# Kernel tuning notes

Hardware: AMD Instinct MI355X
Metric: run time of the kernel (lower is better)

Reference implementation:

```python
import jax, jax.numpy as jnp
import numpy as np

P, A = 8, 65536            # poses, atoms per pose
N = P * A                  # total atoms
N1 = N + 1                 # kin nodes (node 0 = virtual root)


def _local_hts(dofs):
    """Per-node local homogeneous transform from bond DOFs.
    dofs[:,0]=phi (torsion), dofs[:,1]=theta (bond angle), dofs[:,2]=d (length).
    M = Rz(phi) @ Ry(theta) @ Trans_x(d)   (NeRF-style internal coordinates)."""
    phi, theta, d = dofs[:, 0], dofs[:, 1], dofs[:, 2]
    cp, sp = jnp.cos(phi), jnp.sin(phi)
    ct, st = jnp.cos(theta), jnp.sin(theta)
    z = jnp.zeros_like(phi)
    o = jnp.ones_like(phi)
    # R = Rz(phi) @ Ry(theta)
    r00, r01, r02 = cp * ct, -sp, cp * st
    r10, r11, r12 = sp * ct, cp, sp * st
    r20, r21, r22 = -st, z, ct
    # t = R @ [d,0,0]
    t0, t1, t2 = d * r00, d * r10, d * r20
    M = jnp.stack([
        jnp.stack([r00, r01, r02, t0], -1),
        jnp.stack([r10, r11, r12, t1], -1),
        jnp.stack([r20, r21, r22, t2], -1),
        jnp.stack([z, z, z, o], -1),
    ], -2)  # [N1,4,4]
    return M


def setup_inputs() -> dict:
    rng = np.random.default_rng(0)
    # tree: each node's parent is 1..4 nodes back (topologically sorted), root self-parented
    parents = np.zeros(N1, np.int32)
    idx = np.arange(1, N1)
    parents[1:] = np.maximum(idx - 1 - rng.integers(0, 4, size=N), 0).astype(np.int32)
    # kinforest.id: permutation mapping kin node (1..N) -> flat atom index
    kin_id = rng.permutation(N).astype(np.int32)
    # base DOFs (detached full_dofs): realistic bond geometry
    base = np.zeros((N1, 4), np.float32)
    base[:, 1] = rng.uniform(1.5, 2.2, N1)          # theta
    base[:, 2] = rng.normal(1.53, 0.02, N1)         # bond length
    masked = rng.uniform(-np.pi, np.pi, N1).astype(np.float32)  # torsion params
    bond_w = rng.uniform(0.5, 1.5, (P, A - 1)).astype(np.float32)
    pose_coords = np.zeros((P, A, 3), np.float32)
    return {
        "masked_dofs": jnp.asarray(masked),
        "base_dofs": jnp.asarray(base),
        "pose_coords": jnp.asarray(pose_coords),
        "bond_w": jnp.asarray(bond_w),
        "parents": jnp.asarray(parents),
        "kin_id": jnp.asarray(kin_id),
    }


def reference(masked_dofs, base_dofs, pose_coords, bond_w, parents, kin_id):
    # 1) write optimizable DOFs into full DOF tensor (dof_mask = torsion column)
    dofs = base_dofs.at[:, 0].set(masked_dofs)
    # 2) per-node local transforms; root = identity
    M = _local_hts(dofs)
    M = M.at[0].set(jnp.eye(4, dtype=M.dtype))
    # 3) forwardKin: compose parent->child transforms via pointer doubling
    n_iters = int(np.ceil(np.log2(N1)))
    def body(carry, _):
        G, p = carry
        G = jnp.einsum('nij,njk->nik', G[p], G)
        return (G, p[p]), None
    (G, _), _ = jax.lax.scan(body, (M, parents), None, length=n_iters)
    kincoords = G[1:, :3, 3]  # [N,3] global positions (skip root)
    # 4) scatter kin coords back into pose-stack coordinates
    flat = pose_coords.reshape(-1, 3).at[kin_id].set(kincoords)
    coords = flat.reshape(pose_coords.shape)  # [P,A,3]
    # 5) whole-pose scoring: weighted bonded quadratic energy per pose
    d = coords[:, 1:] - coords[:, :-1]
    energy = jnp.sum(bond_w * jnp.sum(d * d, -1), axis=-1)  # [P]
    return energy
```

## Files before the change

kernel.cpp:

```cpp
#include <hip/hip_runtime.h>

#define N_TOT  524288
#define NN1    524289
#define PP     8
#define AA     65536
#define SEGLEN 64
#define NSEG   8193
#define CHUNK  64
#define NCHK   129
#define NE     (NCHK*4)

#define OFF_COORDS 0
#define OFF_NT   2097152
#define OFF_L1G  4194308
#define OFF_L1E  4587572
#define OFF_PREG 4620344
#define OFF_PREE 5013608
#define OFF_CLG  5046380
#define OFF_CLE  5052572

static __device__ __forceinline__ void set_ident(float* a){
  a[0]=1.f;a[1]=0.f;a[2]=0.f;a[3]=0.f;
  a[4]=0.f;a[5]=1.f;a[6]=0.f;a[7]=0.f;
  a[8]=0.f;a[9]=0.f;a[10]=1.f;a[11]=0.f;
}

static __device__ __forceinline__ void compose(const float* Aa, const float* B, float* O){
  #pragma unroll
  for(int r=0;r<3;r++){
    float a0=Aa[r*4+0],a1=Aa[r*4+1],a2=Aa[r*4+2],a3=Aa[r*4+3];
    O[r*4+0]=a0*B[0]+a1*B[4]+a2*B[8];
    O[r*4+1]=a0*B[1]+a1*B[5]+a2*B[9];
    O[r*4+2]=a0*B[2]+a1*B[6]+a2*B[10];
    O[r*4+3]=a0*B[3]+a1*B[7]+a2*B[11]+a3;
  }
}

static __device__ __forceinline__ void load12(const float4* b4, int idx, float* a){
  float4 x=b4[idx*3+0], y=b4[idx*3+1], z=b4[idx*3+2];
  a[0]=x.x;a[1]=x.y;a[2]=x.z;a[3]=x.w;
  a[4]=y.x;a[5]=y.y;a[6]=y.z;a[7]=y.w;
  a[8]=z.x;a[9]=z.y;a[10]=z.z;a[11]=z.w;
}
static __device__ __forceinline__ void store12(float4* b4, int idx, const float* a){
  b4[idx*3+0]=make_float4(a[0],a[1],a[2],a[3]);
  b4[idx*3+1]=make_float4(a[4],a[5],a[6],a[7]);
  b4[idx*3+2]=make_float4(a[8],a[9],a[10],a[11]);
}

static __device__ __forceinline__ void wave_scan(
    int w, int lane,
    const float* __restrict__ masked, const float4* __restrict__ base4,
    const int* __restrict__ parents,
    float G[12], int& pk)
{
  int i0 = w*SEGLEN;
  int i = i0 + lane;
  if(i == 0 || i >= NN1){
    set_ident(G); pk = 0xFF;
  } else {
    float4 b = base4[i];
    float phi = masked[i];
    float sp,cp,st,ct;
    __sincosf(phi,&sp,&cp);
    __sincosf(b.y,&st,&ct);
    float dd = b.z;
    G[0]=cp*ct; G[1]=-sp; G[2]=cp*st; G[3]=dd*G[0];
    G[4]=sp*ct; G[5]=cp;  G[6]=sp*st; G[7]=dd*G[4];
    G[8]=-st;   G[9]=0.f; G[10]=ct;   G[11]=dd*G[8];
    int rel = parents[i] - i0;
    pk = (rel >= 0) ? rel : (((rel+4)<<8) | 0xFF);
  }
  #pragma unroll
  for(int step=0; step<6; ++step){
    int ptr = pk & 0xFF;
    bool act = (ptr != 0xFF);
    int src = act ? ptr : lane;
    float g2[12];
    #pragma unroll
    for(int q=0;q<12;q++) g2[q] = __shfl(G[q], src, 64);
    int pk2 = __shfl(pk, src, 64);
    float ng[12];
    compose(g2, G, ng);
    #pragma unroll
    for(int q=0;q<12;q++) G[q] = act ? ng[q] : G[q];
    pk = act ? pk2 : pk;
  }
}

__global__ __launch_bounds__(1024) void fk1(
    const float* __restrict__ masked, const float4* __restrict__ base4,
    const int* __restrict__ parents,
    float4* __restrict__ L1G, int* __restrict__ L1E,
    float4* __restrict__ NT, float* __restrict__ out)
{
  if(blockIdx.x==0 && threadIdx.x < PP) out[threadIdx.x] = 0.f;
  int w = blockIdx.x*16 + (threadIdx.x>>6);
  if(w >= NSEG) return;
  int lane = threadIdx.x & 63;
  float G[12]; int pk;
  wave_scan(w, lane, masked, base4, parents, G, pk);
  int i = w*SEGLEN + lane;
  int tag = (pk>>8)&3;
  if(i < NN1){
    NT[i] = make_float4(G[3], G[7], G[11], __int_as_float(tag));
  }
  if(lane >= 60){
    int j = lane - 60;
    store12(L1G, w*4+j, G);
    L1E[w*4+j] = tag;
  }
}

__global__ __launch_bounds__(64) void fk2(
    const float4* __restrict__ L1G, const int* __restrict__ L1E,
    float4* __restrict__ PREG, int* __restrict__ PREE,
    float4* __restrict__ CLG, int* __restrict__ CLE)
{
  int g = blockIdx.x;
  int j = threadIdx.x;
  int s0 = g*CHUNK;
  int ns = min(CHUNK, NSEG - s0);
  int sj = s0 + min(j, ns-1);

  float A[4][12]; int at[4];
  #pragma unroll
  for(int t=0;t<4;t++){
    load12(L1G, sj*4+t, A[t]);
    at[t] = L1E[sj*4+t];
  }
  if(j >= ns){
    #pragma unroll
    for(int t=0;t<4;t++){ set_ident(A[t]); at[t]=t; }
  }

  #pragma unroll
  for(int step=0; step<6; ++step){
    int d = 1<<step;
    int src = (j >= d) ? (j - d) : j;
    float f[4][12]; int ft[4];
    #pragma unroll
    for(int t=0;t<4;t++){
      #pragma unroll
      for(int q=0;q<12;q++) f[t][q] = __shfl(A[t][q], src, 64);
      ft[t] = __shfl(at[t], src, 64);
    }
    bool act = (j >= d) && (j < ns);
    float nA[4][12]; int nt[4];
    #pragma unroll
    for(int t=0;t<4;t++){
      int tt = at[t];
      float sel[12];
      #pragma unroll
      for(int q=0;q<12;q++){
        float v01 = (tt&1) ? f[1][q] : f[0][q];
        float v23 = (tt&1) ? f[3][q] : f[2][q];
        sel[q] = (tt&2) ? v23 : v01;
      }
      compose(sel, A[t], nA[t]);
      int t01 = (tt&1) ? ft[1] : ft[0];
      int t23 = (tt&1) ? ft[3] : ft[2];
      nt[t] = (tt&2) ? t23 : t01;
    }
    #pragma unroll
    for(int t=0;t<4;t++){
      #pragma unroll
      for(int q=0;q<12;q++) A[t][q] = act ? nA[t][q] : A[t][q];
      at[t] = act ? nt[t] : at[t];
    }
  }

  if(j == 0){
    float I[12]; set_ident(I);
    #pragma unroll
    for(int t=0;t<4;t++){
      store12(PREG, s0*4+t, I);
      PREE[s0*4+t] = t;
    }
  }
  if(j < ns-1){
    #pragma unroll
    for(int t=0;t<4;t++){
      store12(PREG, (s0+j+1)*4+t, A[t]);
      PREE[(s0+j+1)*4+t] = at[t];
    }
  }
  if(j == ns-1){
    #pragma unroll
    for(int t=0;t<4;t++){
      store12(CLG, g*4+t, A[t]);
      CLE[g*4+t] = at[t];
    }
  }
}

__global__ __launch_bounds__(1024) void fk34(
    const int* __restrict__ kin, const float4* __restrict__ NT,
    const float4* __restrict__ PREG, const int* __restrict__ PREE,
    const float4* __restrict__ CLG, const int* __restrict__ CLE,
    float4* __restrict__ coords)
{
  __shared__ float Lg[NE*12];
  __shared__ int   Le[NE];
  float4* Lg4 = (float4*)Lg;
  int tid = threadIdx.x;

  if(tid < NE){
    float a[12]; load12(CLG, tid, a);
    Lg4[tid*3+0]=make_float4(a[0],a[1],a[2],a[3]);
    Lg4[tid*3+1]=make_float4(a[4],a[5],a[6],a[7]);
    Lg4[tid*3+2]=make_float4(a[8],a[9],a[10],a[11]);
    Le[tid]=CLE[tid];
  }
  __syncthreads();
  for(int d=1; d<NCHK; d<<=1){
    float ng[12]; int ne2=0;
    bool doit = (tid<NE) && ((tid>>2)>=d);
    if(doit){
      int myE = Le[tid];
      int pe = ((tid>>2)-d)*4 + myE;
      float own[12], pg[12];
      load12(Lg4, tid, own);
      load12(Lg4, pe, pg);
      compose(pg, own, ng);
      ne2 = Le[pe];
    }
    __syncthreads();
    if(doit){
      Lg4[tid*3+0]=make_float4(ng[0],ng[1],ng[2],ng[3]);
      Lg4[tid*3+1]=make_float4(ng[4],ng[5],ng[6],ng[7]);
      Lg4[tid*3+2]=make_float4(ng[8],ng[9],ng[10],ng[11]);
      Le[tid]=ne2;
    }
    __syncthreads();
  }

  int w = blockIdx.x*16 + (tid>>6);
  if(w >= NSEG) return;
  int lane = tid & 63;
  int i = w*SEGLEN + lane;
  if(i == 0 || i >= NN1) return;
  float4 nt = NT[i];
  int tag = __float_as_int(nt.w) & 3;
  int c = w >> 6;
  int e = PREE[w*4+tag];
  float bg[12], pg[12], A[12];
  if(c == 0){ set_ident(bg); }
  else { load12(Lg4, (c-1)*4+e, bg); }
  load12(PREG, w*4+tag, pg);
  compose(bg, pg, A);
  float x = A[0]*nt.x + A[1]*nt.y + A[2]*nt.z  + A[3];
  float y = A[4]*nt.x + A[5]*nt.y + A[6]*nt.z  + A[7];
  float z = A[8]*nt.x + A[9]*nt.y + A[10]*nt.z + A[11];
  coords[kin[i-1]] = make_float4(x, y, z, 0.f);
}

__global__ void fk5(const float4* __restrict__ coords, const float* __restrict__ bw,
                    float* __restrict__ out)
{
  int p = blockIdx.x >> 5;
  int sub = blockIdx.x & 31;
  int a0 = sub * 2048;
  int aend = min(a0 + 2048, AA - 1);
  float sum = 0.f;
  for(int a = a0 + (int)threadIdx.x; a < aend; a += 256){
    int r = p*AA + a;
    float4 c0 = coords[r], c1 = coords[r+1];
    float dx = c1.x-c0.x, dy = c1.y-c0.y, dz = c1.z-c0.z;
    sum += bw[p*(AA-1)+a]*(dx*dx+dy*dy+dz*dz);
  }
  #pragma unroll
  for(int off=32;off>0;off>>=1) sum += __shfl_down(sum, off, 64);
  __shared__ float red[4];
  int lane = threadIdx.x & 63, wid = threadIdx.x >> 6;
  if(lane==0) red[wid]=sum;
  __syncthreads();
  if(threadIdx.x==0){
    float tot = red[0]+red[1]+red[2]+red[3];
    atomicAdd(&out[p], tot);
  }
}

extern "C" void kernel_launch(void* const* d_in, const int* in_sizes, int n_in,
                              void* d_out, int out_size, void* d_ws, size_t ws_size,
                              hipStream_t stream)
{
  const float*  masked  = (const float*)d_in[0];
  const float4* base4   = (const float4*)d_in[1];
  const float*  bw      = (const float*)d_in[3];
  const int*    parents = (const int*)d_in[4];
  const int*    kin     = (const int*)d_in[5];

  float* ws = (float*)d_ws;
  float4* coords = (float4*)(ws + OFF_COORDS);
  float4* NT   = (float4*)(ws + OFF_NT);
  float4* L1G  = (float4*)(ws + OFF_L1G);
  int*    L1E  = (int*)(ws + OFF_L1E);
  float4* PREG = (float4*)(ws + OFF_PREG);
  int*    PREE = (int*)(ws + OFF_PREE);
  float4* CLG  = (float4*)(ws + OFF_CLG);
  int*    CLE  = (int*)(ws + OFF_CLE);
  float*  out  = (float*)d_out;

  int nblk = (NSEG + 15) / 16;
  fk1<<<nblk, 1024, 0, stream>>>(masked, base4, parents, L1G, L1E, NT, out);
  fk2<<<NCHK, 64, 0, stream>>>(L1G, L1E, PREG, PREE, CLG, CLE);
  fk34<<<nblk, 1024, 0, stream>>>(kin, NT, PREG, PREE, CLG, CLE, coords);
  fk5<<<PP*32, 256, 0, stream>>>(coords, bw, out);
}
```

Measured before the change: 47.68 us.

## Replace coords scatter with inverse-permutation gather in scoring kernel

Instead of scattering computed positions to permuted atom slots in fk34, positions are written contiguously in kin order and fk1 builds an inverse permutation of kin_id. The scoring kernel then gathers each atom's position through this inverse map, stages it in shared memory, and computes neighbor differences from there, with one block per 1024 atoms. This turns the random 16-byte scatter writes into coalesced writes plus random gathered reads, and removes the duplicate neighbor reads. It adds an extra random int write pass in fk1 and indirect reads in fk5.

```diff
diff --git a/kernel.cpp b/kernel.cpp
--- a/kernel.cpp
+++ b/kernel.cpp
@@ -10,7 +10,7 @@
 #define NCHK   129
 #define NE     (NCHK*4)
 
-#define OFF_COORDS 0
+#define OFF_POS  0
 #define OFF_NT   2097152
 #define OFF_L1G  4194308
 #define OFF_L1E  4587572
@@ -18,6 +18,7 @@
 #define OFF_PREE 5013608
 #define OFF_CLG  5046380
 #define OFF_CLE  5052572
+#define OFF_KINV 5053088
 
 static __device__ __forceinline__ void set_ident(float* a){
   a[0]=1.f;a[1]=0.f;a[2]=0.f;a[3]=0.f;
@@ -90,17 +91,19 @@
 
 __global__ __launch_bounds__(1024) void fk1(
     const float* __restrict__ masked, const float4* __restrict__ base4,
-    const int* __restrict__ parents,
+    const int* __restrict__ parents, const int* __restrict__ kin,
     float4* __restrict__ L1G, int* __restrict__ L1E,
-    float4* __restrict__ NT, float* __restrict__ out)
+    float4* __restrict__ NT, int* __restrict__ kinInv,
+    float* __restrict__ out)
 {
   if(blockIdx.x==0 && threadIdx.x < PP) out[threadIdx.x] = 0.f;
   int w = blockIdx.x*16 + (threadIdx.x>>6);
   if(w >= NSEG) return;
   int lane = threadIdx.x & 63;
+  int i = w*SEGLEN + lane;
+  if(i > 0 && i < NN1) kinInv[kin[i-1]] = i-1;
   float G[12]; int pk;
   wave_scan(w, lane, masked, base4, parents, G, pk);
-  int i = w*SEGLEN + lane;
   int tag = (pk>>8)&3;
   if(i < NN1){
     NT[i] = make_float4(G[3], G[7], G[11], __int_as_float(tag));
@@ -195,10 +198,10 @@
 }
 
 __global__ __launch_bounds__(1024) void fk34(
-    const int* __restrict__ kin, const float4* __restrict__ NT,
+    const float4* __restrict__ NT,
     const float4* __restrict__ PREG, const int* __restrict__ PREE,
     const float4* __restrict__ CLG, const int* __restrict__ CLE,
-    float4* __restrict__ coords)
+    float4* __restrict__ POS)
 {
   __shared__ float Lg[NE*12];
   __shared__ int   Le[NE];
@@ -252,32 +255,43 @@
   float x = A[0]*nt.x + A[1]*nt.y + A[2]*nt.z  + A[3];
   float y = A[4]*nt.x + A[5]*nt.y + A[6]*nt.z  + A[7];
   float z = A[8]*nt.x + A[9]*nt.y + A[10]*nt.z + A[11];
-  coords[kin[i-1]] = make_float4(x, y, z, 0.f);
-}
-
-__global__ void fk5(const float4* __restrict__ coords, const float* __restrict__ bw,
-                    float* __restrict__ out)
-{
-  int p = blockIdx.x >> 5;
-  int sub = blockIdx.x & 31;
-  int a0 = sub * 2048;
-  int aend = min(a0 + 2048, AA - 1);
+  POS[i-1] = make_float4(x, y, z, 0.f);
+}
+
+__global__ __launch_bounds__(1024) void fk5(
+    const float4* __restrict__ POS, const int* __restrict__ kinInv,
+    const float* __restrict__ bw, float* __restrict__ out)
+{
+  __shared__ float sx[1025], sy[1025], sz[1025];
+  __shared__ float red[16];
+  int tid = threadIdx.x;
+  int base = blockIdx.x * 1024;
+  int r = base + tid;
+  float4 p0 = POS[kinInv[r]];
+  sx[tid]=p0.x; sy[tid]=p0.y; sz[tid]=p0.z;
+  if(tid == 0 && base + 1024 < N_TOT){
+    float4 p1 = POS[kinInv[base + 1024]];
+    sx[1024]=p1.x; sy[1024]=p1.y; sz[1024]=p1.z;
+  }
+  __syncthreads();
+  int a = r & (AA-1);
   float sum = 0.f;
-  for(int a = a0 + (int)threadIdx.x; a < aend; a += 256){
-    int r = p*AA + a;
-    float4 c0 = coords[r], c1 = coords[r+1];
-    float dx = c1.x-c0.x, dy = c1.y-c0.y, dz = c1.z-c0.z;
-    sum += bw[p*(AA-1)+a]*(dx*dx+dy*dy+dz*dz);
-  }
-  #pragma unroll
-  for(int off=32;off>0;off>>=1) sum += __shfl_down(sum, off, 64);
-  __shared__ float red[4];
-  int lane = threadIdx.x & 63, wid = threadIdx.x >> 6;
+  if(a != AA-1){
+    float dx = sx[tid+1]-sx[tid];
+    float dy = sy[tid+1]-sy[tid];
+    float dz = sz[tid+1]-sz[tid];
+    sum = bw[(r>>16)*(AA-1) + a]*(dx*dx+dy*dy+dz*dz);
+  }
+  #pragma unroll
+  for(int off=32; off>0; off>>=1) sum += __shfl_down(sum, off, 64);
+  int lane = tid & 63, wid = tid >> 6;
   if(lane==0) red[wid]=sum;
   __syncthreads();
-  if(threadIdx.x==0){
-    float tot = red[0]+red[1]+red[2]+red[3];
-    atomicAdd(&out[p], tot);
+  if(tid==0){
+    float tot=0.f;
+    #pragma unroll
+    for(int q=0;q<16;q++) tot += red[q];
+    atomicAdd(&out[base>>16], tot);
   }
 }
 
@@ -292,19 +306,20 @@
   const int*    kin     = (const int*)d_in[5];
 
   float* ws = (float*)d_ws;
-  float4* coords = (float4*)(ws + OFF_COORDS);
-  float4* NT   = (float4*)(ws + OFF_NT);
-  float4* L1G  = (float4*)(ws + OFF_L1G);
-  int*    L1E  = (int*)(ws + OFF_L1E);
-  float4* PREG = (float4*)(ws + OFF_PREG);
-  int*    PREE = (int*)(ws + OFF_PREE);
-  float4* CLG  = (float4*)(ws + OFF_CLG);
-  int*    CLE  = (int*)(ws + OFF_CLE);
-  float*  out  = (float*)d_out;
+  float4* POS   = (float4*)(ws + OFF_POS);
+  float4* NT    = (float4*)(ws + OFF_NT);
+  float4* L1G   = (float4*)(ws + OFF_L1G);
+  int*    L1E   = (int*)(ws + OFF_L1E);
+  float4* PREG  = (float4*)(ws + OFF_PREG);
+  int*    PREE  = (int*)(ws + OFF_PREE);
+  float4* CLG   = (float4*)(ws + OFF_CLG);
+  int*    CLE   = (int*)(ws + OFF_CLE);
+  int*    kinInv= (int*)(ws + OFF_KINV);
+  float*  out   = (float*)d_out;
 
   int nblk = (NSEG + 15) / 16;
-  fk1<<<nblk, 1024, 0, stream>>>(masked, base4, parents, L1G, L1E, NT, out);
+  fk1<<<nblk, 1024, 0, stream>>>(masked, base4, parents, kin, L1G, L1E, NT, kinInv, out);
   fk2<<<NCHK, 64, 0, stream>>>(L1G, L1E, PREG, PREE, CLG, CLE);
-  fk34<<<nblk, 1024, 0, stream>>>(kin, NT, PREG, PREE, CLG, CLE, coords);
-  fk5<<<PP*32, 256, 0, stream>>>(coords, bw, out);
-}
+  fk34<<<nblk, 1024, 0, stream>>>(NT, PREG, PREE, CLG, CLE, POS);
+  fk5<<<N_TOT/1024, 1024, 0, stream>>>(POS, kinInv, bw, out);
+}
```

Measured after the change: 56.11 us. 17.7% more time.
